# Performance work log

Measured on AMD Instinct MI355X. Metric: run time of the kernel, lower is better.

The kernel has to match this reference:

```python
import jax, jax.numpy as jnp
import numpy as np

GAMMA = 0.99
LMBDA = 0.95
SHAPE = (8192, 256, 4, 1)  # (batch, steps, agents, 1)


def setup_inputs() -> dict:
    key = jax.random.key(0)
    k1, k2, k3, k4 = jax.random.split(key, 4)
    reward = jax.random.normal(k1, SHAPE, dtype=jnp.float32)
    # sparse binary termination flags (as float, matching terminated.float())
    terminated = (jax.random.uniform(k2, SHAPE) < 0.01).astype(jnp.float32)
    value = jax.random.normal(k3, SHAPE, dtype=jnp.float32)
    next_value = jax.random.normal(k4, SHAPE, dtype=jnp.float32)
    return {"reward": reward, "terminated": terminated,
            "value": value, "next_value": next_value}


def _gae(reward, terminated, value, next_value):
    not_done = 1.0 - terminated
    # delta_t = r_t + gamma * V(s_{t+1}) * not_done_t - V(s_t), all steps at once
    delta = reward + GAMMA * next_value * not_done - value  # (B, T, ...)

    # time-major for the scan: (T, B, ...)
    delta_t = jnp.moveaxis(delta, 1, 0)
    nd_t = jnp.moveaxis(not_done, 1, 0)

    def step(gae, x):
        d, nd = x
        gae = d + GAMMA * LMBDA * nd * gae
        return gae, gae

    init = jnp.zeros(delta_t.shape[1:], dtype=delta.dtype)
    # reverse=True: backward-time recurrence, outputs aligned to original order
    _, adv_t = jax.lax.scan(step, init, (delta_t, nd_t), reverse=True)
    advantages = jnp.moveaxis(adv_t, 0, 1)  # back to (B, T, ...)
    returns = advantages + value
    return advantages, returns


def reference(reward, terminated, value, next_value):
    return _gae(reward, terminated, value, next_value)
```

## Files before the change

kernel.cpp:

```cpp
#include <hip/hip_runtime.h>


#define GAMMA 0.99f
#define LMBDA 0.95f

constexpr int T = 256;

__global__ __launch_bounds__(256, 5) void gae_scan_kernel(
    const float* __restrict__ reward,
    const float* __restrict__ terminated,
    const float* __restrict__ value,
    const float* __restrict__ next_value,
    float* __restrict__ adv_out,
    float* __restrict__ ret_out)
{
    __shared__ float bufD[4][16 * 64];
    __shared__ float bufC[4][16 * 64];

    const int w    = threadIdx.x >> 6;
    const int lane = threadIdx.x & 63;
    const int b    = blockIdx.x * 4 + w;

    float* __restrict__ D_ = bufD[w];
    float* __restrict__ C_ = bufC[w];

    float4 v4[4];
#pragma unroll
    for (int q = 0; q < 4; ++q) {
        const int f  = 64 * q + lane;
        const int gi = b * 256 + f;
        const float4 r  = ((const float4*)reward)[gi];
        const float4 tm = ((const float4*)terminated)[gi];
        const float4 v  = ((const float4*)value)[gi];
        const float4 nv = ((const float4*)next_value)[gi];
        v4[q] = v;

        const int s    = 255 - f;
        const int row  = s & 15;
        const int col  = (4 * (s >> 4) + 4 * row) & 63;
        const int addr = row * 64 + col;

        float4 d4, c4;
        d4.x = r.x + GAMMA * nv.x * (1.0f - tm.x) - v.x;
        d4.y = r.y + GAMMA * nv.y * (1.0f - tm.y) - v.y;
        d4.z = r.z + GAMMA * nv.z * (1.0f - tm.z) - v.z;
        d4.w = r.w + GAMMA * nv.w * (1.0f - tm.w) - v.w;
        c4.x = (GAMMA * LMBDA) * (1.0f - tm.x);
        c4.y = (GAMMA * LMBDA) * (1.0f - tm.y);
        c4.z = (GAMMA * LMBDA) * (1.0f - tm.z);
        c4.w = (GAMMA * LMBDA) * (1.0f - tm.w);
        *((float4*)&D_[addr]) = d4;
        *((float4*)&C_[addr]) = c4;
    }
    __syncthreads();

    const int tc = lane >> 2;
    const int a  = lane & 3;

    float d[16], c[16];
#pragma unroll
    for (int j = 0; j < 16; ++j) {
        const int col = (4 * tc + 4 * j + a) & 63;
        d[j] = D_[j * 64 + col];
        c[j] = C_[j * 64 + col];
    }

    float D = d[0], K = c[0];
#pragma unroll
    for (int j = 1; j < 16; ++j) { D = d[j] + c[j] * D; K = c[j] * K; }

#pragma unroll
    for (int s2 = 1; s2 < 16; s2 <<= 1) {
        const float pD = __shfl_up(D, (unsigned)(4 * s2), 64);
        const float pK = __shfl_up(K, (unsigned)(4 * s2), 64);
        if (tc >= s2) { D = D + K * pD; K = K * pK; }
    }

    float x = __shfl_up(D, 4u, 64);
    if (tc == 0) x = 0.0f;

    float g = x;
#pragma unroll
    for (int j = 0; j < 16; ++j) {
        g = d[j] + c[j] * g;
        const int col = (4 * tc + 4 * j + a) & 63;
        D_[j * 64 + col] = g;
    }
    __syncthreads();

#pragma unroll
    for (int q = 0; q < 4; ++q) {
        const int f   = 64 * q + lane;
        const int s   = 255 - f;
        const int row = s & 15;
        const int col = (4 * (s >> 4) + 4 * row) & 63;
        const float4 g4 = *((const float4*)&D_[row * 64 + col]);

        const int gi = b * 256 + f;
        ((float4*)adv_out)[gi] = g4;
        float4 rt;
        rt.x = g4.x + v4[q].x;
        rt.y = g4.y + v4[q].y;
        rt.z = g4.z + v4[q].z;
        rt.w = g4.w + v4[q].w;
        ((float4*)ret_out)[gi] = rt;
    }
}

extern "C" void kernel_launch(void* const* d_in, const int* in_sizes, int n_in,
                              void* d_out, int out_size, void* d_ws, size_t ws_size,
                              hipStream_t stream) {
    const float* reward     = (const float*)d_in[0];
    const float* terminated = (const float*)d_in[1];
    const float* value      = (const float*)d_in[2];
    const float* next_value = (const float*)d_in[3];

    const int B = 8192;
    const int n_elem = B * T * 4;
    float* adv = (float*)d_out;
    float* ret = adv + n_elem;

    gae_scan_kernel<<<B / 4, 256, 0, stream>>>(reward, terminated, value,
                                               next_value, adv, ret);
}
```

Measured before the change: 179.1 us.

## Pack done flag into delta LSB, use wave fences and nontemporal stores

Stores the not-done flag in the low mantissa bit of delta, so a single LDS buffer replaces the two D and C buffers, halving shared memory and allowing occupancy to rise from 5 to 8 blocks. Each wave now uses only its own LDS slice, so the block-wide barriers become workgroup fences. Outputs are written with nontemporal stores. Clearing the delta LSB perturbs values by about one ulp, and a fence without a barrier relies on wave-private LDS access.

```diff
diff --git a/kernel.cpp b/kernel.cpp
--- a/kernel.cpp
+++ b/kernel.cpp
@@ -3,10 +3,17 @@
 
 #define GAMMA 0.99f
 #define LMBDA 0.95f
+#define GL    (0.99f * 0.95f)
 
 constexpr int T = 256;
 
-__global__ __launch_bounds__(256, 5) void gae_scan_kernel(
+typedef float vfloat4 __attribute__((ext_vector_type(4)));
+
+static __device__ __forceinline__ void wave_lds_fence() {
+    __builtin_amdgcn_fence(__ATOMIC_SEQ_CST, "workgroup");
+}
+
+__global__ __launch_bounds__(256, 8) void gae_scan_kernel(
     const float* __restrict__ reward,
     const float* __restrict__ terminated,
     const float* __restrict__ value,
@@ -14,45 +21,38 @@
     float* __restrict__ adv_out,
     float* __restrict__ ret_out)
 {
-    __shared__ float bufD[4][16 * 64];
-    __shared__ float bufC[4][16 * 64];
+    __shared__ float buf[4][16 * 64];
 
     const int w    = threadIdx.x >> 6;
     const int lane = threadIdx.x & 63;
     const int b    = blockIdx.x * 4 + w;
+    float* __restrict__ P = buf[w];
 
-    float* __restrict__ D_ = bufD[w];
-    float* __restrict__ C_ = bufC[w];
-
-    float4 v4[4];
+    vfloat4 v4[4];
 #pragma unroll
     for (int q = 0; q < 4; ++q) {
         const int f  = 64 * q + lane;
         const int gi = b * 256 + f;
-        const float4 r  = ((const float4*)reward)[gi];
-        const float4 tm = ((const float4*)terminated)[gi];
-        const float4 v  = ((const float4*)value)[gi];
-        const float4 nv = ((const float4*)next_value)[gi];
+        const vfloat4 r  = ((const vfloat4*)reward)[gi];
+        const vfloat4 tm = ((const vfloat4*)terminated)[gi];
+        const vfloat4 v  = ((const vfloat4*)value)[gi];
+        const vfloat4 nv = ((const vfloat4*)next_value)[gi];
         v4[q] = v;
 
-        const int s    = 255 - f;
-        const int row  = s & 15;
-        const int col  = (4 * (s >> 4) + 4 * row) & 63;
-        const int addr = row * 64 + col;
+        const int s   = 255 - f;
+        const int row = s & 15;
+        const int col = (4 * (s >> 4) + 4 * row) & 63;
 
-        float4 d4, c4;
-        d4.x = r.x + GAMMA * nv.x * (1.0f - tm.x) - v.x;
-        d4.y = r.y + GAMMA * nv.y * (1.0f - tm.y) - v.y;
-        d4.z = r.z + GAMMA * nv.z * (1.0f - tm.z) - v.z;
-        d4.w = r.w + GAMMA * nv.w * (1.0f - tm.w) - v.w;
-        c4.x = (GAMMA * LMBDA) * (1.0f - tm.x);
-        c4.y = (GAMMA * LMBDA) * (1.0f - tm.y);
-        c4.z = (GAMMA * LMBDA) * (1.0f - tm.z);
-        c4.w = (GAMMA * LMBDA) * (1.0f - tm.w);
-        *((float4*)&D_[addr]) = d4;
-        *((float4*)&C_[addr]) = c4;
+        vfloat4 p;
+#pragma unroll
+        for (int c0 = 0; c0 < 4; ++c0) {
+            float dd = r[c0] + GAMMA * nv[c0] * (1.0f - tm[c0]) - v[c0];
+            p[c0] = __uint_as_float((__float_as_uint(dd) & ~1u) |
+                                    (tm[c0] == 0.0f ? 1u : 0u));
+        }
+        *((vfloat4*)&P[row * 64 + col]) = p;
     }
-    __syncthreads();
+    wave_lds_fence();
 
     const int tc = lane >> 2;
     const int a  = lane & 3;
@@ -61,8 +61,9 @@
 #pragma unroll
     for (int j = 0; j < 16; ++j) {
         const int col = (4 * tc + 4 * j + a) & 63;
-        d[j] = D_[j * 64 + col];
-        c[j] = C_[j * 64 + col];
+        const unsigned u = __float_as_uint(P[j * 64 + col]);
+        c[j] = (u & 1u) ? GL : 0.0f;
+        d[j] = __uint_as_float(u & ~1u);
     }
 
     float D = d[0], K = c[0];
@@ -84,9 +85,9 @@
     for (int j = 0; j < 16; ++j) {
         g = d[j] + c[j] * g;
         const int col = (4 * tc + 4 * j + a) & 63;
-        D_[j * 64 + col] = g;
+        P[j * 64 + col] = g;
     }
-    __syncthreads();
+    wave_lds_fence();
 
 #pragma unroll
     for (int q = 0; q < 4; ++q) {
@@ -94,16 +95,12 @@
         const int s   = 255 - f;
         const int row = s & 15;
         const int col = (4 * (s >> 4) + 4 * row) & 63;
-        const float4 g4 = *((const float4*)&D_[row * 64 + col]);
+        const vfloat4 g4 = *((const vfloat4*)&P[row * 64 + col]);
 
         const int gi = b * 256 + f;
-        ((float4*)adv_out)[gi] = g4;
-        float4 rt;
-        rt.x = g4.x + v4[q].x;
-        rt.y = g4.y + v4[q].y;
-        rt.z = g4.z + v4[q].z;
-        rt.w = g4.w + v4[q].w;
-        ((float4*)ret_out)[gi] = rt;
+        __builtin_nontemporal_store(g4, &((vfloat4*)adv_out)[gi]);
+        const vfloat4 rt = g4 + v4[q];
+        __builtin_nontemporal_store(rt, &((vfloat4*)ret_out)[gi]);
     }
 }
 
```

Measured after the change: 188.8 us. +5.4%, slower.
